# Kernel optimization log

Measured on AMD Instinct MI355X. Metric: run time of the kernel, lower is better.

## Reference

```python
import jax, jax.numpy as jnp
import numpy as np

VOCAB, EMB, HID = 32000, 32, 256
B, T = 64, 2048


def setup_inputs() -> dict:
    key = jax.random.key(0)
    ks = jax.random.split(key, 7)
    x = jax.random.randint(ks[0], (B, T), 0, VOCAB, dtype=jnp.int64) if jax.config.jax_enable_x64 else jax.random.randint(ks[0], (B, T), 0, VOCAB, dtype=jnp.int32)
    lengths = jax.random.randint(ks[1], (B,), 1, T + 1, dtype=x.dtype)
    emb = jax.random.normal(ks[2], (VOCAB, EMB), dtype=jnp.float32) * 0.02
    emb = emb.at[0].set(0.0)  # padding_idx = 0
    s = 1.0 / np.sqrt(HID)
    W_ih = jax.random.uniform(ks[3], (4 * HID, EMB), jnp.float32, -s, s)
    W_hh = jax.random.uniform(ks[4], (4 * HID, HID), jnp.float32, -s, s)
    b_ih = jax.random.uniform(ks[5], (4 * HID,), jnp.float32, -s, s)
    b_hh = jax.random.uniform(ks[6], (4 * HID,), jnp.float32, -s, s)
    return {"x": x, "lengths": lengths, "emb": emb, "W_ih": W_ih,
            "W_hh": W_hh, "b_ih": b_ih, "b_hh": b_hh}


def _rnn(xe, mask, W_ih, W_hh, b_ih, b_hh):
    # xe: [B, T, EMB]; mask: [B, T] float (1 = valid, 0 = pad)
    Bm, Tm = xe.shape[0], xe.shape[1]
    h0 = jnp.zeros((Bm, HID), xe.dtype)
    c0 = jnp.zeros((Bm, HID), xe.dtype)

    def step(carry, inp):
        h, c = carry
        x_t, m_t = inp  # [B, EMB], [B, 1]
        gates = x_t @ W_ih.T + b_ih + h @ W_hh.T + b_hh  # [B, 4H]
        i, f, g, o = jnp.split(gates, 4, axis=-1)
        i = jax.nn.sigmoid(i)
        f = jax.nn.sigmoid(f)
        g = jnp.tanh(g)
        o = jax.nn.sigmoid(o)
        c_new = f * c + i * g
        h_new = o * jnp.tanh(c_new)
        # masked state update: padded steps keep previous state
        h = m_t * h_new + (1.0 - m_t) * h
        c = m_t * c_new + (1.0 - m_t) * c
        return (h, c), h

    xs = (jnp.swapaxes(xe, 0, 1), jnp.swapaxes(mask, 0, 1)[..., None])
    (_, _), hs = jax.lax.scan(step, (h0, c0), xs)
    return jnp.swapaxes(hs, 0, 1)  # [B, T, HID]


def reference(x, lengths, emb, W_ih, W_hh, b_ih, b_hh):
    xe = emb[x]  # [B, T, EMB]
    mask = (jnp.arange(x.shape[1])[None, :] < lengths[:, None]).astype(xe.dtype)
    out = _rnn(xe, mask, W_ih, W_hh, b_ih, b_hh)  # [B, T, HID]
    last = out[:, -1, :]  # due to mask-freeze, equals state at each length
    return last[:, None, :]  # [B, 1, HID]
```

## Files before the change

kernel.cpp:

```cpp
#include <hip/hip_runtime.h>
#include <hip/hip_fp16.h>

#define EMB 32
#define HID 256
#define BATCH 64
#define TT  2048

typedef _Float16 half8_t __attribute__((ext_vector_type(8)));
typedef _Float16 half2_t __attribute__((ext_vector_type(2)));

#define W_BYTES  (2*36*512*16)
#define BIAS_OFF W_BYTES
#define ACK_OFF  (BIAS_OFF + 4096)
#define FAST_OFF (ACK_OFF + 1024)


__device__ __forceinline__ float fdot2(half2_t a, half2_t b, float c) {
#if __has_builtin(__builtin_amdgcn_fdot2)
    return __builtin_amdgcn_fdot2(a, b, c, false);
#else
    return c + (float)a[0] * (float)b[0] + (float)a[1] * (float)b[1];
#endif
}

__device__ __forceinline__ float dot8(half8_t w, half8_t x, float acc) {
    acc = fdot2(half2_t{w[0], w[1]}, half2_t{x[0], x[1]}, acc);
    acc = fdot2(half2_t{w[2], w[3]}, half2_t{x[2], x[3]}, acc);
    acc = fdot2(half2_t{w[4], w[5]}, half2_t{x[4], x[5]}, acc);
    acc = fdot2(half2_t{w[6], w[7]}, half2_t{x[6], x[7]}, acc);
    return acc;
}

__device__ __forceinline__ float rcp_fast(float v) {
#if __has_builtin(__builtin_amdgcn_rcpf)
    return __builtin_amdgcn_rcpf(v);
#else
    return 1.0f / v;
#endif
}
__device__ __forceinline__ float sigmoid_fast(float v) {
    return rcp_fast(1.0f + __expf(-v));
}
__device__ __forceinline__ float tanh_fast(float v) {
    v = fminf(fmaxf(v, -15.0f), 15.0f);
    float e = __expf(2.0f * v);
    return (e - 1.0f) * rcp_fast(e + 1.0f);
}

__device__ __forceinline__ void barrier_lds() {
    asm volatile("s_waitcnt lgkmcnt(0)\n\ts_barrier" ::: "memory");
}

__device__ __forceinline__ float quad_reduce(float v) {
    int t = __builtin_amdgcn_mov_dpp(__float_as_int(v), 0xB1, 0xF, 0xF, true);
    v += __int_as_float(t);
    t = __builtin_amdgcn_mov_dpp(__float_as_int(v), 0x4E, 0xF, 0xF, true);
    v += __int_as_float(t);
    return v;
}

__device__ __forceinline__ unsigned int load_fast(const unsigned int* p) {
    return *(volatile const unsigned int*)p;
}
__device__ __forceinline__ unsigned int load_slow(const unsigned int* p) {
    return __hip_atomic_load(p, __ATOMIC_RELAXED, __HIP_MEMORY_SCOPE_AGENT);
}

__device__ __forceinline__ int gate_row(int r, int Q) {
    return r == 0 ? Q : r == 1 ? 256 + Q : r == 2 ? 512 + Q : 768 + Q;
}

__global__ void prep_kernel(const float* __restrict__ W_ih,
                            const float* __restrict__ W_hh,
                            const float* __restrict__ b_ih,
                            const float* __restrict__ b_hh,
                            char* __restrict__ ws,
                            unsigned int* __restrict__ outw) {
    int bid = blockIdx.x, t = threadIdx.x;
    if (bid < 72) {
        int R = bid / 36, c = bid % 36;
        int r = c / 9, jj = c % 9;
        int Q = 128 * R + (t >> 2), l = t & 3;
        int row = gate_row(r, Q);
        half8_t v;
#pragma unroll
        for (int e = 0; e < 8; ++e) {
            int p = 8 * jj + e;
            float f;
            if (p < 8)       f = W_ih[row * EMB + 8 * l + p];
            else if (p < 40) f = W_hh[row * HID + 128 * R + 32 * l + (p - 8)];
            else             f = W_hh[row * HID + 128 * (1 - R) + 32 * l + (p - 40)];
            v[e] = (_Float16)f;
        }
        ((half8_t*)ws)[((size_t)bid) * 512 + t] = v;
    } else if (bid == 72) {
        float* bias = (float*)(ws + BIAS_OFF);
        for (int i = t; i < 1024; i += 512) {
            int Q = i >> 2, r = i & 3;
            int row = gate_row(r, Q);
            bias[i] = b_ih[row] + b_hh[row];
        }
    } else if (bid < 105) {
        int g = (bid - 73) * 512 + t;
        outw[g] = ((g >> 6) & 1) ? 0x00010001u : 0u;
    } else {
        int g = (bid - 105) * 512 + t;
        ((unsigned int*)(ws + FAST_OFF))[g] = ((g >> 6) & 1) ? 0x00010001u : 0u;
    }
}

__global__ __launch_bounds__(512, 2) void rnn_kernel(const int* __restrict__ x,
                                                     const int* __restrict__ lengths,
                                                     const float* __restrict__ emb,
                                                     char* __restrict__ ws,
                                                     float* __restrict__ out_) {
    __shared__ __align__(16) _Float16 xhbuf[2][320];

    const int bid  = blockIdx.x;
    const int role = bid >> 6;
    const int b    = bid & 63;
    const int tid  = threadIdx.x;
    const int q    = tid >> 2;
    const int l    = tid & 3;
    const int Q    = 128 * role + q;

    half8_t w[4][9];
    {
        const half8_t* Wp = (const half8_t*)ws + (size_t)role * 36 * 512;
#pragma unroll
        for (int r = 0; r < 4; ++r)
#pragma unroll
            for (int jj = 0; jj < 9; ++jj) w[r][jj] = Wp[(r * 9 + jj) * 512 + tid];
    }
    float4 bs = *(const float4*)(ws + BIAS_OFF + (size_t)Q * 16);

    unsigned int* sexch = (unsigned int*)out_ + (size_t)b * 256;
    unsigned int* fexch = (unsigned int*)(ws + FAST_OFF) + (size_t)b * 256;
    unsigned int* smine = sexch + role * 128;
    unsigned int* spart = sexch + (1 - role) * 128;
    unsigned int* fmine = fexch + role * 128;
    unsigned int* fpart = fexch + (1 - role) * 128;

    int L = lengths[b];
    if (L > TT) L = TT;
    if (L < 1) L = 1;
    const int* __restrict__ xb = x + b * TT;

    if (tid < 320) xhbuf[0][tid] = (_Float16)0.0f;
    __syncthreads();
    if (tid < EMB) {
        float e0 = emb[xb[0] * EMB + tid];
        xhbuf[0][72 * (tid >> 3) + (tid & 7)] = (_Float16)e0;
    }
    __syncthreads();

    float cc = 0.0f, hh = 0.0f;

    float p0 = 0.f, p1 = 0.f, p2 = 0.f, p3 = 0.f;
    {
        const _Float16* cur = xhbuf[0];
        half8_t xv[5];
#pragma unroll
        for (int jj = 0; jj < 5; ++jj) xv[jj] = *(const half8_t*)(cur + 72 * l + 8 * jj);
#pragma unroll
        for (int jj = 0; jj < 5; ++jj) {
            p0 = dot8(w[0][jj], xv[jj], p0);
            p1 = dot8(w[1][jj], xv[jj], p1);
            p2 = dot8(w[2][jj], xv[jj], p2);
            p3 = dot8(w[3][jj], xv[jj], p3);
        }
    }

    int mode = 0;

#pragma unroll 1
    for (int t = 0; t < L; ++t) {
        const _Float16* __restrict__ cur = xhbuf[t & 1];
        _Float16* __restrict__ nxt = xhbuf[(t + 1) & 1];

        float ev = 0.0f;
        if (tid >= 64 && tid < 64 + EMB) {
            int nt = (t + 1 < L) ? xb[t + 1] : 0;
            ev = emb[nt * EMB + (tid - 64)];
        }

        float a0 = p0, a1 = p1, a2 = p2, a3 = p3;
        {
            half8_t xv[4];
#pragma unroll
            for (int jj = 0; jj < 4; ++jj)
                xv[jj] = *(const half8_t*)(cur + 72 * l + 40 + 8 * jj);
#pragma unroll
            for (int jj = 0; jj < 4; ++jj) {
                a0 = dot8(w[0][5 + jj], xv[jj], a0);
                a1 = dot8(w[1][5 + jj], xv[jj], a1);
                a2 = dot8(w[2][5 + jj], xv[jj], a2);
                a3 = dot8(w[3][5 + jj], xv[jj], a3);
            }
        }

        a0 = quad_reduce(a0);
        a1 = quad_reduce(a1);
        a2 = quad_reduce(a2);
        a3 = quad_reduce(a3);
        float iv = sigmoid_fast(a0 + bs.x);
        float fv = sigmoid_fast(a1 + bs.y);
        float gv = tanh_fast(a2 + bs.z);
        float ov = sigmoid_fast(a3 + bs.w);
        cc = fv * cc + iv * gv;
        hh = ov * tanh_fast(cc);

        const unsigned int tg = ((unsigned)(t + 1) >> 1) & 1u;
        const int ps_ = (t + 1) & 1;

        _Float16 hf = (_Float16)hh;
        unsigned short hb = __builtin_bit_cast(unsigned short, hf);
        unsigned int tb = (unsigned int)((hb & 0xFFFEu) | tg);
        unsigned int nb = (unsigned int)__builtin_amdgcn_mov_dpp((int)tb, 0x104, 0xF, 0xF, true);
        if ((tid & 7) == 0) {
            unsigned int dw = tb | (nb << 16);
            int o = ps_ * 64 + (tid >> 3);
            __hip_atomic_store(fmine + o, dw, __ATOMIC_RELAXED, __HIP_MEMORY_SCOPE_WORKGROUP);
            __hip_atomic_store(smine + o, dw, __ATOMIC_RELAXED, __HIP_MEMORY_SCOPE_AGENT);
        }

        if (l == 0) nxt[72 * (q >> 5) + 8 + (q & 31)] = hf;
        if (tid >= 64 && tid < 64 + EMB) {
            int k = tid - 64;
            nxt[72 * (k >> 3) + (k & 7)] = (_Float16)ev;
        }
        barrier_lds();

        unsigned int fdw = 0;
        const unsigned int* fp = fpart + ps_ * 64 + tid;
        const unsigned int* sp = spart + ps_ * 64 + tid;
        if (tid < 64) fdw = mode ? load_slow(sp) : load_fast(fp);

        p0 = 0.f; p1 = 0.f; p2 = 0.f; p3 = 0.f;
        {
            half8_t xv[5];
#pragma unroll
            for (int jj = 0; jj < 5; ++jj)
                xv[jj] = *(const half8_t*)(nxt + 72 * l + 8 * jj);
#pragma unroll
            for (int jj = 0; jj < 5; ++jj) {
                p0 = dot8(w[0][jj], xv[jj], p0);
                p1 = dot8(w[1][jj], xv[jj], p1);
                p2 = dot8(w[2][jj], xv[jj], p2);
                p3 = dot8(w[3][jj], xv[jj], p3);
            }
        }

        if (tid < 64) {
            unsigned int dw = fdw;
            int tries = 0;
            while (!__all(((dw & 1u) == tg) && (((dw >> 16) & 1u) == tg))) {
                ++tries;
                if (mode == 0 && tries > 12) mode = 1;
                if (tries > (1 << 20)) break;
                if (mode) { __builtin_amdgcn_s_sleep(1); dw = load_slow(sp); }
                else      dw = load_fast(fp);
            }
            unsigned short h0 = (unsigned short)(dw & 0xFFFEu);
            unsigned short h1 = (unsigned short)((dw >> 16) & 0xFFFEu);
            int j0 = 2 * tid, j1 = 2 * tid + 1;
            nxt[72 * (j0 >> 5) + 40 + (j0 & 31)] = __builtin_bit_cast(_Float16, h0);
            nxt[72 * (j1 >> 5) + 40 + (j1 & 31)] = __builtin_bit_cast(_Float16, h1);
        }
        barrier_lds();
    }

    int* ack = (int*)(ws + ACK_OFF);
    if (tid == 0)
        __hip_atomic_store(&ack[bid], L, __ATOMIC_RELEASE, __HIP_MEMORY_SCOPE_AGENT);
    if (tid == 0) {
        int tries = 0;
        while (__hip_atomic_load(&ack[bid ^ 64], __ATOMIC_ACQUIRE, __HIP_MEMORY_SCOPE_AGENT) != L) {
            if (++tries > (1 << 20)) break;
            __builtin_amdgcn_s_sleep(8);
        }
    }
    __syncthreads();
    if (l == 0) out_[(size_t)b * 256 + 128 * role + q] = hh;
}

extern "C" void kernel_launch(void* const* d_in, const int* in_sizes, int n_in,
                              void* d_out, int out_size, void* d_ws, size_t ws_size,
                              hipStream_t stream) {
    const int*   x       = (const int*)d_in[0];
    const int*   lengths = (const int*)d_in[1];
    const float* emb     = (const float*)d_in[2];
    const float* W_ih    = (const float*)d_in[3];
    const float* W_hh    = (const float*)d_in[4];
    const float* b_ih    = (const float*)d_in[5];
    const float* b_hh    = (const float*)d_in[6];

    prep_kernel<<<137, 512, 0, stream>>>(W_ih, W_hh, b_ih, b_hh,
                                         (char*)d_ws, (unsigned int*)d_out);
    rnn_kernel<<<128, 512, 0, stream>>>(x, lengths, emb, (char*)d_ws, (float*)d_out);
}
```

Baseline: 2.460 ms.

## Run each batch row in one workgroup with weights split between registers and LDS

Each batch row's recurrence previously ran on two cooperating 512-thread workgroups that swapped half of the hidden state through global memory with flag polling. Now a single 256-thread workgroup handles the whole row. Each thread keeps three quarters of its weight slices in registers (108 half8 vectors) and reads the remaining quarter, plus the bias, from LDS every step. This drops the cross-workgroup handshake and global-memory polling in favour of a plain barrier, at the cost of heavy register pressure (possible spills), extra LDS weight reads per step, and half as many workgroups.

```diff
diff --git a/kernel.cpp b/kernel.cpp
--- a/kernel.cpp
+++ b/kernel.cpp
@@ -3,17 +3,21 @@
 
 #define EMB 32
 #define HID 256
-#define BATCH 64
 #define TT  2048
 
 typedef _Float16 half8_t __attribute__((ext_vector_type(8)));
 typedef _Float16 half2_t __attribute__((ext_vector_type(2)));
 
-#define W_BYTES  (2*36*512*16)
-#define BIAS_OFF W_BYTES
-#define ACK_OFF  (BIAS_OFF + 4096)
-#define FAST_OFF (ACK_OFF + 1024)
-
+
+#define REGW_SLOTS 108
+#define LDSW_SLOTS 36
+#define LDSW_OFF  (REGW_SLOTS * 256 * 16)
+#define BIAS_OFF  (LDSW_OFF + LDSW_SLOTS * 256 * 16)
+
+#define SM_WL    0
+#define SM_BIAS  (LDSW_SLOTS * 256 * 16)
+#define SM_XH    (SM_BIAS + 4096)
+#define SM_BYTES (SM_XH + 2 * 320 * 2 + 64)
 
 __device__ __forceinline__ float fdot2(half2_t a, half2_t b, float c) {
 #if __has_builtin(__builtin_amdgcn_fdot2)
@@ -47,10 +51,6 @@
     return (e - 1.0f) * rcp_fast(e + 1.0f);
 }
 
-__device__ __forceinline__ void barrier_lds() {
-    asm volatile("s_waitcnt lgkmcnt(0)\n\ts_barrier" ::: "memory");
-}
-
 __device__ __forceinline__ float quad_reduce(float v) {
     int t = __builtin_amdgcn_mov_dpp(__float_as_int(v), 0xB1, 0xF, 0xF, true);
     v += __int_as_float(t);
@@ -59,229 +59,153 @@
     return v;
 }
 
-__device__ __forceinline__ unsigned int load_fast(const unsigned int* p) {
-    return *(volatile const unsigned int*)p;
-}
-__device__ __forceinline__ unsigned int load_slow(const unsigned int* p) {
-    return __hip_atomic_load(p, __ATOMIC_RELAXED, __HIP_MEMORY_SCOPE_AGENT);
-}
-
-__device__ __forceinline__ int gate_row(int r, int Q) {
-    return r == 0 ? Q : r == 1 ? 256 + Q : r == 2 ? 512 + Q : 768 + Q;
-}
-
 __global__ void prep_kernel(const float* __restrict__ W_ih,
                             const float* __restrict__ W_hh,
                             const float* __restrict__ b_ih,
                             const float* __restrict__ b_hh,
-                            char* __restrict__ ws,
-                            unsigned int* __restrict__ outw) {
-    int bid = blockIdx.x, t = threadIdx.x;
-    if (bid < 72) {
-        int R = bid / 36, c = bid % 36;
-        int r = c / 9, jj = c % 9;
-        int Q = 128 * R + (t >> 2), l = t & 3;
-        int row = gate_row(r, Q);
+                            char* __restrict__ ws) {
+    int bid = blockIdx.x, t = threadIdx.x, q = t >> 2, l = t & 3;
+    if (bid < REGW_SLOTS + LDSW_SLOTS) {
+        int k = bid;
+        int r, jj, u;
+        if (k < REGW_SLOTS) {
+            int s = k / 36, m = k % 36;
+            r = m / 9; jj = m % 9; u = q + 64 * s;
+        } else {
+            int m = k - REGW_SLOTS;
+            r = m / 9; jj = m % 9; u = q + 192;
+        }
+        int row = r * HID + u;
         half8_t v;
 #pragma unroll
         for (int e = 0; e < 8; ++e) {
-            int p = 8 * jj + e;
-            float f;
-            if (p < 8)       f = W_ih[row * EMB + 8 * l + p];
-            else if (p < 40) f = W_hh[row * HID + 128 * R + 32 * l + (p - 8)];
-            else             f = W_hh[row * HID + 128 * (1 - R) + 32 * l + (p - 40)];
+            int p = 72 * l + 8 * jj + e;
+            float f = (p < EMB) ? W_ih[row * EMB + p]
+                                : W_hh[row * HID + (p - EMB)];
             v[e] = (_Float16)f;
         }
-        ((half8_t*)ws)[((size_t)bid) * 512 + t] = v;
-    } else if (bid == 72) {
-        float* bias = (float*)(ws + BIAS_OFF);
-        for (int i = t; i < 1024; i += 512) {
-            int Q = i >> 2, r = i & 3;
-            int row = gate_row(r, Q);
-            bias[i] = b_ih[row] + b_hh[row];
-        }
-    } else if (bid < 105) {
-        int g = (bid - 73) * 512 + t;
-        outw[g] = ((g >> 6) & 1) ? 0x00010001u : 0u;
+        ((half8_t*)ws)[(size_t)k * 256 + t] = v;
     } else {
-        int g = (bid - 105) * 512 + t;
-        ((unsigned int*)(ws + FAST_OFF))[g] = ((g >> 6) & 1) ? 0x00010001u : 0u;
-    }
-}
-
-__global__ __launch_bounds__(512, 2) void rnn_kernel(const int* __restrict__ x,
+        if (t < 256) {
+            float* bias = (float*)(ws + BIAS_OFF);
+#pragma unroll
+            for (int r = 0; r < 4; ++r)
+                bias[t * 4 + r] = 0.25f * (b_ih[r * HID + t] + b_hh[r * HID + t]);
+        }
+    }
+}
+
+__global__ __launch_bounds__(256, 1) void rnn_kernel(const int* __restrict__ x,
                                                      const int* __restrict__ lengths,
                                                      const float* __restrict__ emb,
-                                                     char* __restrict__ ws,
+                                                     const char* __restrict__ ws,
                                                      float* __restrict__ out_) {
-    __shared__ __align__(16) _Float16 xhbuf[2][320];
-
-    const int bid  = blockIdx.x;
-    const int role = bid >> 6;
-    const int b    = bid & 63;
-    const int tid  = threadIdx.x;
-    const int q    = tid >> 2;
-    const int l    = tid & 3;
-    const int Q    = 128 * role + q;
-
-    half8_t w[4][9];
+    extern __shared__ char smem[];
+    half8_t*  WL = (half8_t*)(smem + SM_WL);
+    float*    BL = (float*)(smem + SM_BIAS);
+    _Float16* XH = (_Float16*)(smem + SM_XH);
+
+    const int b = blockIdx.x, tid = threadIdx.x;
+    const int q = tid >> 2, l = tid & 3;
+
+    half8_t w[REGW_SLOTS];
     {
-        const half8_t* Wp = (const half8_t*)ws + (size_t)role * 36 * 512;
-#pragma unroll
-        for (int r = 0; r < 4; ++r)
-#pragma unroll
-            for (int jj = 0; jj < 9; ++jj) w[r][jj] = Wp[(r * 9 + jj) * 512 + tid];
-    }
-    float4 bs = *(const float4*)(ws + BIAS_OFF + (size_t)Q * 16);
-
-    unsigned int* sexch = (unsigned int*)out_ + (size_t)b * 256;
-    unsigned int* fexch = (unsigned int*)(ws + FAST_OFF) + (size_t)b * 256;
-    unsigned int* smine = sexch + role * 128;
-    unsigned int* spart = sexch + (1 - role) * 128;
-    unsigned int* fmine = fexch + role * 128;
-    unsigned int* fpart = fexch + (1 - role) * 128;
-
+        const half8_t* Wr = (const half8_t*)ws;
+#pragma unroll
+        for (int k = 0; k < REGW_SLOTS; ++k) w[k] = Wr[(size_t)k * 256 + tid];
+    }
+    {
+        const half8_t* Wg = (const half8_t*)(ws + LDSW_OFF);
+        for (int m = tid; m < LDSW_SLOTS * 256; m += 256) WL[m] = Wg[m];
+        const float* bg = (const float*)(ws + BIAS_OFF);
+        for (int i = tid; i < 1024; i += 256) BL[i] = bg[i];
+        for (int i = tid; i < 640; i += 256) XH[i] = (_Float16)0.0f;
+    }
     int L = lengths[b];
     if (L > TT) L = TT;
     if (L < 1) L = 1;
     const int* __restrict__ xb = x + b * TT;
-
-    if (tid < 320) xhbuf[0][tid] = (_Float16)0.0f;
     __syncthreads();
-    if (tid < EMB) {
-        float e0 = emb[xb[0] * EMB + tid];
-        xhbuf[0][72 * (tid >> 3) + (tid & 7)] = (_Float16)e0;
-    }
+    if (tid < EMB) XH[tid] = (_Float16)emb[xb[0] * EMB + tid];
     __syncthreads();
 
-    float cc = 0.0f, hh = 0.0f;
-
-    float p0 = 0.f, p1 = 0.f, p2 = 0.f, p3 = 0.f;
-    {
-        const _Float16* cur = xhbuf[0];
-        half8_t xv[5];
-#pragma unroll
-        for (int jj = 0; jj < 5; ++jj) xv[jj] = *(const half8_t*)(cur + 72 * l + 8 * jj);
-#pragma unroll
-        for (int jj = 0; jj < 5; ++jj) {
-            p0 = dot8(w[0][jj], xv[jj], p0);
-            p1 = dot8(w[1][jj], xv[jj], p1);
-            p2 = dot8(w[2][jj], xv[jj], p2);
-            p3 = dot8(w[3][jj], xv[jj], p3);
-        }
-    }
-
-    int mode = 0;
+    float cs0 = 0.f, cs1 = 0.f, cs2 = 0.f, cs3 = 0.f;
+    float hs0 = 0.f, hs1 = 0.f, hs2 = 0.f, hs3 = 0.f;
 
 #pragma unroll 1
     for (int t = 0; t < L; ++t) {
-        const _Float16* __restrict__ cur = xhbuf[t & 1];
-        _Float16* __restrict__ nxt = xhbuf[(t + 1) & 1];
-
-        float ev = 0.0f;
-        if (tid >= 64 && tid < 64 + EMB) {
+        const _Float16* __restrict__ cur = XH + (t & 1) * 320;
+        _Float16* __restrict__ nxt = XH + ((t + 1) & 1) * 320;
+
+        float ev = 0.f;
+        if (tid < EMB) {
             int nt = (t + 1 < L) ? xb[t + 1] : 0;
-            ev = emb[nt * EMB + (tid - 64)];
-        }
-
-        float a0 = p0, a1 = p1, a2 = p2, a3 = p3;
-        {
-            half8_t xv[4];
-#pragma unroll
-            for (int jj = 0; jj < 4; ++jj)
-                xv[jj] = *(const half8_t*)(cur + 72 * l + 40 + 8 * jj);
-#pragma unroll
-            for (int jj = 0; jj < 4; ++jj) {
-                a0 = dot8(w[0][5 + jj], xv[jj], a0);
-                a1 = dot8(w[1][5 + jj], xv[jj], a1);
-                a2 = dot8(w[2][5 + jj], xv[jj], a2);
-                a3 = dot8(w[3][5 + jj], xv[jj], a3);
+            ev = emb[nt * EMB + tid];
+        }
+
+        float a[16];
+#pragma unroll
+        for (int s = 0; s < 4; ++s) {
+            const float4 bb = *(const float4*)(BL + 4 * (q + 64 * s));
+            a[4 * s + 0] = bb.x; a[4 * s + 1] = bb.y;
+            a[4 * s + 2] = bb.z; a[4 * s + 3] = bb.w;
+        }
+
+#pragma unroll
+        for (int jj = 0; jj < 9; ++jj) {
+            const half8_t xv = *(const half8_t*)(cur + 72 * l + 8 * jj);
+#pragma unroll
+            for (int s = 0; s < 3; ++s)
+#pragma unroll
+                for (int r = 0; r < 4; ++r)
+                    a[4 * s + r] = dot8(w[s * 36 + r * 9 + jj], xv, a[4 * s + r]);
+#pragma unroll
+            for (int r = 0; r < 4; ++r) {
+                const half8_t wv = WL[(r * 9 + jj) * 256 + tid];
+                a[12 + r] = dot8(wv, xv, a[12 + r]);
             }
         }
 
-        a0 = quad_reduce(a0);
-        a1 = quad_reduce(a1);
-        a2 = quad_reduce(a2);
-        a3 = quad_reduce(a3);
-        float iv = sigmoid_fast(a0 + bs.x);
-        float fv = sigmoid_fast(a1 + bs.y);
-        float gv = tanh_fast(a2 + bs.z);
-        float ov = sigmoid_fast(a3 + bs.w);
-        cc = fv * cc + iv * gv;
-        hh = ov * tanh_fast(cc);
-
-        const unsigned int tg = ((unsigned)(t + 1) >> 1) & 1u;
-        const int ps_ = (t + 1) & 1;
-
-        _Float16 hf = (_Float16)hh;
-        unsigned short hb = __builtin_bit_cast(unsigned short, hf);
-        unsigned int tb = (unsigned int)((hb & 0xFFFEu) | tg);
-        unsigned int nb = (unsigned int)__builtin_amdgcn_mov_dpp((int)tb, 0x104, 0xF, 0xF, true);
-        if ((tid & 7) == 0) {
-            unsigned int dw = tb | (nb << 16);
-            int o = ps_ * 64 + (tid >> 3);
-            __hip_atomic_store(fmine + o, dw, __ATOMIC_RELAXED, __HIP_MEMORY_SCOPE_WORKGROUP);
-            __hip_atomic_store(smine + o, dw, __ATOMIC_RELAXED, __HIP_MEMORY_SCOPE_AGENT);
-        }
-
-        if (l == 0) nxt[72 * (q >> 5) + 8 + (q & 31)] = hf;
-        if (tid >= 64 && tid < 64 + EMB) {
-            int k = tid - 64;
-            nxt[72 * (k >> 3) + (k & 7)] = (_Float16)ev;
-        }
-        barrier_lds();
-
-        unsigned int fdw = 0;
-        const unsigned int* fp = fpart + ps_ * 64 + tid;
-        const unsigned int* sp = spart + ps_ * 64 + tid;
-        if (tid < 64) fdw = mode ? load_slow(sp) : load_fast(fp);
-
-        p0 = 0.f; p1 = 0.f; p2 = 0.f; p3 = 0.f;
-        {
-            half8_t xv[5];
-#pragma unroll
-            for (int jj = 0; jj < 5; ++jj)
-                xv[jj] = *(const half8_t*)(nxt + 72 * l + 8 * jj);
-#pragma unroll
-            for (int jj = 0; jj < 5; ++jj) {
-                p0 = dot8(w[0][jj], xv[jj], p0);
-                p1 = dot8(w[1][jj], xv[jj], p1);
-                p2 = dot8(w[2][jj], xv[jj], p2);
-                p3 = dot8(w[3][jj], xv[jj], p3);
-            }
-        }
-
-        if (tid < 64) {
-            unsigned int dw = fdw;
-            int tries = 0;
-            while (!__all(((dw & 1u) == tg) && (((dw >> 16) & 1u) == tg))) {
-                ++tries;
-                if (mode == 0 && tries > 12) mode = 1;
-                if (tries > (1 << 20)) break;
-                if (mode) { __builtin_amdgcn_s_sleep(1); dw = load_slow(sp); }
-                else      dw = load_fast(fp);
-            }
-            unsigned short h0 = (unsigned short)(dw & 0xFFFEu);
-            unsigned short h1 = (unsigned short)((dw >> 16) & 0xFFFEu);
-            int j0 = 2 * tid, j1 = 2 * tid + 1;
-            nxt[72 * (j0 >> 5) + 40 + (j0 & 31)] = __builtin_bit_cast(_Float16, h0);
-            nxt[72 * (j1 >> 5) + 40 + (j1 & 31)] = __builtin_bit_cast(_Float16, h1);
-        }
-        barrier_lds();
-    }
-
-    int* ack = (int*)(ws + ACK_OFF);
-    if (tid == 0)
-        __hip_atomic_store(&ack[bid], L, __ATOMIC_RELEASE, __HIP_MEMORY_SCOPE_AGENT);
-    if (tid == 0) {
-        int tries = 0;
-        while (__hip_atomic_load(&ack[bid ^ 64], __ATOMIC_ACQUIRE, __HIP_MEMORY_SCOPE_AGENT) != L) {
-            if (++tries > (1 << 20)) break;
-            __builtin_amdgcn_s_sleep(8);
-        }
-    }
-    __syncthreads();
-    if (l == 0) out_[(size_t)b * 256 + 128 * role + q] = hh;
+#pragma unroll
+        for (int i = 0; i < 16; ++i) a[i] = quad_reduce(a[i]);
+
+        {
+            float iv = sigmoid_fast(a[0]),  fv = sigmoid_fast(a[1]);
+            float gv = tanh_fast(a[2]),     ov = sigmoid_fast(a[3]);
+            cs0 = fv * cs0 + iv * gv; hs0 = ov * tanh_fast(cs0);
+        }
+        {
+            float iv = sigmoid_fast(a[4]),  fv = sigmoid_fast(a[5]);
+            float gv = tanh_fast(a[6]),     ov = sigmoid_fast(a[7]);
+            cs1 = fv * cs1 + iv * gv; hs1 = ov * tanh_fast(cs1);
+        }
+        {
+            float iv = sigmoid_fast(a[8]),  fv = sigmoid_fast(a[9]);
+            float gv = tanh_fast(a[10]),    ov = sigmoid_fast(a[11]);
+            cs2 = fv * cs2 + iv * gv; hs2 = ov * tanh_fast(cs2);
+        }
+        {
+            float iv = sigmoid_fast(a[12]), fv = sigmoid_fast(a[13]);
+            float gv = tanh_fast(a[14]),    ov = sigmoid_fast(a[15]);
+            cs3 = fv * cs3 + iv * gv; hs3 = ov * tanh_fast(cs3);
+        }
+
+        if (l == 0) {
+            nxt[32 + q]       = (_Float16)hs0;
+            nxt[32 + q + 64]  = (_Float16)hs1;
+            nxt[32 + q + 128] = (_Float16)hs2;
+            nxt[32 + q + 192] = (_Float16)hs3;
+        }
+        if (tid < EMB) nxt[tid] = (_Float16)ev;
+        __syncthreads();
+    }
+
+    if (l == 0) {
+        out_[(size_t)b * HID + q]       = hs0;
+        out_[(size_t)b * HID + q + 64]  = hs1;
+        out_[(size_t)b * HID + q + 128] = hs2;
+        out_[(size_t)b * HID + q + 192] = hs3;
+    }
 }
 
 extern "C" void kernel_launch(void* const* d_in, const int* in_sizes, int n_in,
@@ -295,7 +219,15 @@
     const float* b_ih    = (const float*)d_in[5];
     const float* b_hh    = (const float*)d_in[6];
 
-    prep_kernel<<<137, 512, 0, stream>>>(W_ih, W_hh, b_ih, b_hh,
-                                         (char*)d_ws, (unsigned int*)d_out);
-    rnn_kernel<<<128, 512, 0, stream>>>(x, lengths, emb, (char*)d_ws, (float*)d_out);
-}
+    static bool attr_done = false;
+    if (!attr_done) {
+        (void)hipFuncSetAttribute((const void*)rnn_kernel,
+                                  hipFuncAttributeMaxDynamicSharedMemorySize,
+                                  SM_BYTES);
+        attr_done = true;
+    }
+
+    prep_kernel<<<145, 256, 0, stream>>>(W_ih, W_hh, b_ih, b_hh, (char*)d_ws);
+    rnn_kernel<<<64, 256, SM_BYTES, stream>>>(x, lengths, emb,
+                                              (const char*)d_ws, (float*)d_out);
+}
```

Measured after the change: 6.076 ms. +147.0%, slower.

## Drop fast exchange path, prefetch embeddings two steps ahead, tune polling

Applied to the files above, without the earlier changes.

Removes the second workgroup-scoped exchange buffer and its volatile fast-path polling. The two paired blocks now exchange hidden-state halves only through the agent-scope buffer, polling tightly and sleeping only after many tries. The embedding row for step t+2 is now loaded one iteration earlier, so global-memory latency overlaps more of the recurrence. It also sets launch bounds to one block per CU and initializes the ack array to -1, trading fewer per-step stores for possibly slower coherent loads.

```diff
diff --git a/kernel.cpp b/kernel.cpp
--- a/kernel.cpp
+++ b/kernel.cpp
@@ -12,7 +12,6 @@
 #define W_BYTES  (2*36*512*16)
 #define BIAS_OFF W_BYTES
 #define ACK_OFF  (BIAS_OFF + 4096)
-#define FAST_OFF (ACK_OFF + 1024)
 
 
 __device__ __forceinline__ float fdot2(half2_t a, half2_t b, float c) {
@@ -59,9 +58,6 @@
     return v;
 }
 
-__device__ __forceinline__ unsigned int load_fast(const unsigned int* p) {
-    return *(volatile const unsigned int*)p;
-}
 __device__ __forceinline__ unsigned int load_slow(const unsigned int* p) {
     return __hip_atomic_load(p, __ATOMIC_RELAXED, __HIP_MEMORY_SCOPE_AGENT);
 }
@@ -100,16 +96,14 @@
             int row = gate_row(r, Q);
             bias[i] = b_ih[row] + b_hh[row];
         }
-    } else if (bid < 105) {
+        if (t < 128) ((int*)(ws + ACK_OFF))[t] = -1;
+    } else {
         int g = (bid - 73) * 512 + t;
         outw[g] = ((g >> 6) & 1) ? 0x00010001u : 0u;
-    } else {
-        int g = (bid - 105) * 512 + t;
-        ((unsigned int*)(ws + FAST_OFF))[g] = ((g >> 6) & 1) ? 0x00010001u : 0u;
-    }
-}
-
-__global__ __launch_bounds__(512, 2) void rnn_kernel(const int* __restrict__ x,
+    }
+}
+
+__global__ __launch_bounds__(512, 1) void rnn_kernel(const int* __restrict__ x,
                                                      const int* __restrict__ lengths,
                                                      const float* __restrict__ emb,
                                                      char* __restrict__ ws,
@@ -119,6 +113,7 @@
     const int bid  = blockIdx.x;
     const int role = bid >> 6;
     const int b    = bid & 63;
+    const int pbid = bid ^ 64;
     const int tid  = threadIdx.x;
     const int q    = tid >> 2;
     const int l    = tid & 3;
@@ -135,11 +130,8 @@
     float4 bs = *(const float4*)(ws + BIAS_OFF + (size_t)Q * 16);
 
     unsigned int* sexch = (unsigned int*)out_ + (size_t)b * 256;
-    unsigned int* fexch = (unsigned int*)(ws + FAST_OFF) + (size_t)b * 256;
     unsigned int* smine = sexch + role * 128;
     unsigned int* spart = sexch + (1 - role) * 128;
-    unsigned int* fmine = fexch + role * 128;
-    unsigned int* fpart = fexch + (1 - role) * 128;
 
     int L = lengths[b];
     if (L > TT) L = TT;
@@ -171,17 +163,21 @@
         }
     }
 
-    int mode = 0;
+    float ev = 0.f;
+    if (tid >= 64 && tid < 64 + EMB) {
+        int nt = (1 < L) ? xb[1] : 0;
+        ev = emb[nt * EMB + (tid - 64)];
+    }
 
 #pragma unroll 1
     for (int t = 0; t < L; ++t) {
         const _Float16* __restrict__ cur = xhbuf[t & 1];
         _Float16* __restrict__ nxt = xhbuf[(t + 1) & 1];
 
-        float ev = 0.0f;
+        float ev2 = 0.0f;
         if (tid >= 64 && tid < 64 + EMB) {
-            int nt = (t + 1 < L) ? xb[t + 1] : 0;
-            ev = emb[nt * EMB + (tid - 64)];
+            int nt2 = (t + 2 < L) ? xb[t + 2] : 0;
+            ev2 = emb[nt2 * EMB + (tid - 64)];
         }
 
         float a0 = p0, a1 = p1, a2 = p2, a3 = p3;
@@ -218,10 +214,9 @@
         unsigned int tb = (unsigned int)((hb & 0xFFFEu) | tg);
         unsigned int nb = (unsigned int)__builtin_amdgcn_mov_dpp((int)tb, 0x104, 0xF, 0xF, true);
         if ((tid & 7) == 0) {
-            unsigned int dw = tb | (nb << 16);
+            unsigned int dwv = tb | (nb << 16);
             int o = ps_ * 64 + (tid >> 3);
-            __hip_atomic_store(fmine + o, dw, __ATOMIC_RELAXED, __HIP_MEMORY_SCOPE_WORKGROUP);
-            __hip_atomic_store(smine + o, dw, __ATOMIC_RELAXED, __HIP_MEMORY_SCOPE_AGENT);
+            __hip_atomic_store(smine + o, dwv, __ATOMIC_RELAXED, __HIP_MEMORY_SCOPE_AGENT);
         }
 
         if (l == 0) nxt[72 * (q >> 5) + 8 + (q & 31)] = hf;
@@ -232,9 +227,8 @@
         barrier_lds();
 
         unsigned int fdw = 0;
-        const unsigned int* fp = fpart + ps_ * 64 + tid;
         const unsigned int* sp = spart + ps_ * 64 + tid;
-        if (tid < 64) fdw = mode ? load_slow(sp) : load_fast(fp);
+        if (tid < 64) fdw = load_slow(sp);
 
         p0 = 0.f; p1 = 0.f; p2 = 0.f; p3 = 0.f;
         {
@@ -255,11 +249,9 @@
             unsigned int dw = fdw;
             int tries = 0;
             while (!__all(((dw & 1u) == tg) && (((dw >> 16) & 1u) == tg))) {
-                ++tries;
-                if (mode == 0 && tries > 12) mode = 1;
-                if (tries > (1 << 20)) break;
-                if (mode) { __builtin_amdgcn_s_sleep(1); dw = load_slow(sp); }
-                else      dw = load_fast(fp);
+                if (++tries > (1 << 20)) break;
+                if (tries > 512) __builtin_amdgcn_s_sleep(2);
+                dw = load_slow(sp);
             }
             unsigned short h0 = (unsigned short)(dw & 0xFFFEu);
             unsigned short h1 = (unsigned short)((dw >> 16) & 0xFFFEu);
@@ -268,6 +260,8 @@
             nxt[72 * (j1 >> 5) + 40 + (j1 & 31)] = __builtin_bit_cast(_Float16, h1);
         }
         barrier_lds();
+
+        ev = ev2;
     }
 
     int* ack = (int*)(ws + ACK_OFF);
@@ -275,7 +269,7 @@
         __hip_atomic_store(&ack[bid], L, __ATOMIC_RELEASE, __HIP_MEMORY_SCOPE_AGENT);
     if (tid == 0) {
         int tries = 0;
-        while (__hip_atomic_load(&ack[bid ^ 64], __ATOMIC_ACQUIRE, __HIP_MEMORY_SCOPE_AGENT) != L) {
+        while (__hip_atomic_load(&ack[pbid], __ATOMIC_ACQUIRE, __HIP_MEMORY_SCOPE_AGENT) != L) {
             if (++tries > (1 << 20)) break;
             __builtin_amdgcn_s_sleep(8);
         }
@@ -295,7 +289,7 @@
     const float* b_ih    = (const float*)d_in[5];
     const float* b_hh    = (const float*)d_in[6];
 
-    prep_kernel<<<137, 512, 0, stream>>>(W_ih, W_hh, b_ih, b_hh,
+    prep_kernel<<<105, 512, 0, stream>>>(W_ih, W_hh, b_ih, b_hh,
                                          (char*)d_ws, (unsigned int*)d_out);
     rnn_kernel<<<128, 512, 0, stream>>>(x, lengths, emb, (char*)d_ws, (float*)d_out);
 }
```

Result: slower. 2.514 ms (+2.2%).
